# Kernel optimization log

Measured on AMD Instinct MI355X. Metric: run time of the kernel, lower is better.

The kernel has to match this reference:

```python
import jax, jax.numpy as jnp
import numpy as np

N_NODES = 100000
N_EDGES = 1600000
IN_CH = 128
HID = 64
N_LAYER = 4
N_CLASS = 10
N_GRAPHS = 512
EPS = 1e-5


def setup_inputs() -> dict:
    key = jax.random.key(0)
    ks = jax.random.split(key, 20)
    x = jax.random.normal(ks[0], (N_NODES, IN_CH), dtype=jnp.float32)
    src = jax.random.randint(ks[1], (N_EDGES,), 0, N_NODES)
    dst = jax.random.randint(ks[2], (N_EDGES,), 0, N_NODES)
    batch = jnp.sort(jax.random.randint(ks[3], (N_NODES,), 0, N_GRAPHS))
    s = 0.05
    W0 = jax.random.normal(ks[4], (IN_CH, HID), dtype=jnp.float32) * s
    Ws = jax.random.normal(ks[5], (N_LAYER - 1, HID, HID), dtype=jnp.float32) * s
    bs = jax.random.normal(ks[6], (N_LAYER, HID), dtype=jnp.float32) * s
    g_bn = jnp.ones((N_LAYER, HID), dtype=jnp.float32)
    b_bn = jnp.zeros((N_LAYER, HID), dtype=jnp.float32)
    m3 = 3 * N_LAYER * HID  # 768
    m2 = 2 * N_LAYER * HID  # 512
    m1 = N_LAYER * HID      # 256
    g_out = jnp.ones((m3,), dtype=jnp.float32)
    b_out = jnp.zeros((m3,), dtype=jnp.float32)
    w1 = jax.random.normal(ks[7], (m3, m2), dtype=jnp.float32) * s
    b1 = jnp.zeros((m2,), dtype=jnp.float32)
    w2 = jax.random.normal(ks[8], (m2, m1), dtype=jnp.float32) * s
    b2 = jnp.zeros((m1,), dtype=jnp.float32)
    w3 = jax.random.normal(ks[9], (m1, N_CLASS), dtype=jnp.float32) * s
    b3 = jnp.zeros((N_CLASS,), dtype=jnp.float32)
    return dict(x=x, src=src, dst=dst, batch=batch, W0=W0, Ws=Ws, bs=bs,
                g_bn=g_bn, b_bn=b_bn, g_out=g_out, b_out=b_out,
                w1=w1, b1=b1, w2=w2, b2=b2, w3=w3, b3=b3)


def _bn(h, g, b):
    # training-mode BatchNorm1d over rows (biased variance, as torch normalizes)
    m = jnp.mean(h, axis=0)
    v = jnp.var(h, axis=0)
    return (h - m) * jax.lax.rsqrt(v + EPS) * g + b


def reference(x, src, dst, batch, W0, Ws, bs, g_bn, b_bn, g_out, b_out,
              w1, b1, w2, b2, w3, b3):
    n = x.shape[0]
    loops = jnp.arange(n)
    s = jnp.concatenate([src, loops])  # self-loops (GCNConv)
    d = jnp.concatenate([dst, loops])
    deg = jax.ops.segment_sum(jnp.ones_like(s, dtype=x.dtype), d, num_segments=n)
    norm = jax.lax.rsqrt(jnp.maximum(deg, 1.0))
    coef = (norm[s] * norm[d])[:, None]

    def conv(h, W, bias):
        h = h @ W
        msg = h[s] * coef  # [E+N, HID] gather
        return jax.ops.segment_sum(msg, d, num_segments=n) + bias

    H = []
    h = conv(x, W0, bs[0])           # conv_act is identity (default)
    h = _bn(h, g_bn[0], b_bn[0])
    H.append(h)
    for i in range(N_LAYER - 1):
        h = conv(h, Ws[i], bs[i + 1])
        h = _bn(h, g_bn[i + 1], b_bn[i + 1])
        H.append(h)
    H = jnp.concatenate(H, axis=1)   # [N, n_layer*HID]

    # mean / add / max pooling by graph id
    add = jax.ops.segment_sum(H, batch, num_segments=N_GRAPHS)
    cnt = jax.ops.segment_sum(jnp.ones((n,), H.dtype), batch, num_segments=N_GRAPHS)
    avg = add / jnp.maximum(cnt, 1.0)[:, None]
    mx = jax.ops.segment_max(H, batch, num_segments=N_GRAPHS)
    mx = jnp.where(cnt[:, None] > 0, mx, 0.0)
    Hg = jnp.concatenate([avg, add, mx], axis=1)  # [G, 3*n_layer*HID]

    # funnel readout (dropout p=0 -> identity)
    z = _bn(Hg, g_out, b_out)
    z = jax.nn.relu(z @ w1 + b1)
    z = jax.nn.relu(z @ w2 + b2)
    return jax.nn.log_softmax(z @ w3 + b3, axis=1)
```

## Files before the change

kernel.cpp:

```cpp
#include <hip/hip_runtime.h>
#include <hip/hip_bf16.h>
#include <math.h>

#define HIDC 64
#define NLAYER 4
#define NG 512
#define M3 768
#define M2 512
#define M1 256
#define NCLS 10
#define EPSV 1e-5f
#define NB 512
#define EPT 16
#define NPW 4

__device__ inline unsigned bf16rne(float x){
  unsigned u = __float_as_uint(x);
  return (u + 0x7fffu + ((u >> 16) & 1u)) >> 16;
}
__device__ inline unsigned packbf2(float lo, float hi){
  return bf16rne(lo) | (bf16rne(hi) << 16);
}
__device__ inline float blo(unsigned u){ return __uint_as_float(u << 16); }
__device__ inline float bhi(unsigned u){ return __uint_as_float(u & 0xffff0000u); }

__global__ __launch_bounds__(256) void k_bhist(const int* __restrict__ dst, int E,
                                               int* __restrict__ bcnt){
  __shared__ int lc[NB];
  int tid = threadIdx.x;
  for (int i = tid; i < NB; i += 256) lc[i] = 0;
  __syncthreads();
  for (int e = blockIdx.x*256 + tid; e < E; e += gridDim.x*256)
    atomicAdd(&lc[__builtin_nontemporal_load(&dst[e]) >> 8], 1);
  __syncthreads();
  for (int i = tid; i < NB; i += 256){
    int c = lc[i];
    if (c) atomicAdd(&bcnt[i], c);
  }
}

__global__ void k_bscan(const int* __restrict__ bcnt, int* __restrict__ bofs,
                        int* __restrict__ bcursor){
  __shared__ int tmp[NB];
  int tid = threadIdx.x;
  int v = bcnt[tid];
  tmp[tid] = v; __syncthreads();
  for (int ofs = 1; ofs < NB; ofs <<= 1){
    int t = (tid >= ofs) ? tmp[tid-ofs] : 0;
    __syncthreads();
    tmp[tid] += t;
    __syncthreads();
  }
  int ex = tmp[tid] - v;
  bofs[tid] = ex;
  bcursor[tid] = ex;
}

__global__ __launch_bounds__(256) void k_bscatter(const int* __restrict__ src,
    const int* __restrict__ dst, int E, int* __restrict__ bcursor, int2* __restrict__ stage){
  __shared__ int lcnt[NB];
  __shared__ int lbase[NB];
  int tid = threadIdx.x;
  int t0 = blockIdx.x*(256*EPT);
  for (int i = tid; i < NB; i += 256) lcnt[i] = 0;
  __syncthreads();
  int s_[EPT], d_[EPT];
  bool ok[EPT];
  #pragma unroll
  for (int i = 0; i < EPT; i++){
    int e = t0 + i*256 + tid;
    ok[i] = (e < E);
    int ee = ok[i] ? e : 0;
    d_[i] = __builtin_nontemporal_load(&dst[ee]);
    s_[i] = __builtin_nontemporal_load(&src[ee]);
    if (ok[i]) atomicAdd(&lcnt[d_[i] >> 8], 1);
  }
  __syncthreads();
  for (int i = tid; i < NB; i += 256){
    int c = lcnt[i];
    lbase[i] = c ? atomicAdd(&bcursor[i], c) : 0;
  }
  __syncthreads();
  #pragma unroll
  for (int i = 0; i < EPT; i++){
    if (ok[i]){
      int pos = atomicAdd(&lbase[d_[i] >> 8], 1);
      stage[pos] = make_int2(s_[i], d_[i]);
    }
  }
}

__global__ __launch_bounds__(256) void k_deg_b(const int2* __restrict__ stage,
    const int* __restrict__ bofs, const int* __restrict__ bcnt,
    int* __restrict__ row_start, int* __restrict__ cursor,
    float* __restrict__ normv, int n, int E){
  __shared__ int hist[256];
  __shared__ int tmp[256];
  int b = blockIdx.x;
  int tid = threadIdx.x;
  hist[tid] = 0;
  __syncthreads();
  int st = bofs[b], en = st + bcnt[b];
  for (int i = st + tid; i < en; i += 256)
    atomicAdd(&hist[stage[i].y & 255], 1);
  __syncthreads();
  int v = hist[tid];
  tmp[tid] = v;
  __syncthreads();
  for (int o = 1; o < 256; o <<= 1){
    int t = (tid >= o) ? tmp[tid-o] : 0;
    __syncthreads();
    tmp[tid] += t;
    __syncthreads();
  }
  int node = b*256 + tid;
  if (node < n){
    int rs = st + tmp[tid] - v;
    row_start[node] = rs;
    cursor[node] = rs;
    normv[node] = rsqrtf((float)(v + 1));
  }
  if (b == 0 && tid == 0) row_start[n] = E;
}

__global__ __launch_bounds__(256) void k_fill_b(const int2* __restrict__ stage,
    const int* __restrict__ bofs, const int* __restrict__ bcnt,
    int* __restrict__ cursor, int* __restrict__ col){
  int b = blockIdx.x;
  int st = bofs[b], en = st + bcnt[b];
  for (int i = st + threadIdx.x; i < en; i += 256){
    int2 p = stage[i];
    int pos = atomicAdd(&cursor[p.y], 1);
    col[pos] = p.x;
  }
}

__global__ __launch_bounds__(256) void k_gemm_l0(const float* __restrict__ A,
    const float* __restrict__ W, const float* __restrict__ norm,
    unsigned* __restrict__ U32, int n){
  __shared__ float Wl[128*64];
  __shared__ float Al[128*36];
  int tid = threadIdx.x;
  {
    const float4* W4 = (const float4*)W;
    float4* Wl4 = (float4*)Wl;
    for (int i = tid; i < 128*16; i += 256) Wl4[i] = W4[i];
  }
  int rb = blockIdx.x * 128;
  int cg = tid & 7;
  int rg = tid >> 3;
  float acc[4][8];
  #pragma unroll
  for (int i = 0; i < 4; i++)
    #pragma unroll
    for (int c = 0; c < 8; c++) acc[i][c] = 0.f;
  for (int kc = 0; kc < 128; kc += 32){
    __syncthreads();
    {
      int r = tid >> 1, h = tid & 1;
      int rr = rb + r; if (rr >= n) rr = 0;
      const float* Ag = A + (size_t)rr*128 + kc + h*16;
      float4 v0 = *(const float4*)(Ag+0);
      float4 v1 = *(const float4*)(Ag+4);
      float4 v2 = *(const float4*)(Ag+8);
      float4 v3 = *(const float4*)(Ag+12);
      float* dl = &Al[r*36 + h*16];
      *(float4*)(dl+0) = v0; *(float4*)(dl+4) = v1;
      *(float4*)(dl+8) = v2; *(float4*)(dl+12) = v3;
    }
    __syncthreads();
    #pragma unroll
    for (int kk = 0; kk < 32; kk += 4){
      float4 a0 = *(const float4*)&Al[(rg*4+0)*36 + kk];
      float4 a1 = *(const float4*)&Al[(rg*4+1)*36 + kk];
      float4 a2 = *(const float4*)&Al[(rg*4+2)*36 + kk];
      float4 a3 = *(const float4*)&Al[(rg*4+3)*36 + kk];
      float ar[4][4] = {{a0.x,a0.y,a0.z,a0.w},{a1.x,a1.y,a1.z,a1.w},
                        {a2.x,a2.y,a2.z,a2.w},{a3.x,a3.y,a3.z,a3.w}};
      #pragma unroll
      for (int j = 0; j < 4; j++){
        const float* wr = &Wl[(kc+kk+j)*64 + cg*8];
        float4 w0 = *(const float4*)(wr);
        float4 w1 = *(const float4*)(wr+4);
        float wv[8] = {w0.x,w0.y,w0.z,w0.w,w1.x,w1.y,w1.z,w1.w};
        #pragma unroll
        for (int i = 0; i < 4; i++)
          #pragma unroll
          for (int c = 0; c < 8; c++)
            acc[i][c] += ar[i][j]*wv[c];
      }
    }
  }
  #pragma unroll
  for (int i = 0; i < 4; i++){
    int r = rb + rg*4 + i;
    if (r < n){
      float nr = norm[r];
      uint4 o;
      o.x = packbf2(acc[i][0]*nr, acc[i][1]*nr);
      o.y = packbf2(acc[i][2]*nr, acc[i][3]*nr);
      o.z = packbf2(acc[i][4]*nr, acc[i][5]*nr);
      o.w = packbf2(acc[i][6]*nr, acc[i][7]*nr);
      *(uint4*)(U32 + (size_t)r*32 + cg*4) = o;
    }
  }
}

__global__ __launch_bounds__(256) void k_gemm_lb(const unsigned* __restrict__ Ab,
    const float* __restrict__ W, const float* __restrict__ norm,
    const float* __restrict__ scsh, unsigned* __restrict__ U32, int n){
  __shared__ float Wl[64*64];
  __shared__ float Al[128*36];
  __shared__ float ss[128];
  int tid = threadIdx.x;
  {
    const float4* W4 = (const float4*)W;
    float4* Wl4 = (float4*)Wl;
    for (int i = tid; i < 64*16; i += 256) Wl4[i] = W4[i];
  }
  if (tid < 128) ss[tid] = scsh[tid];
  int rb = blockIdx.x * 128;
  int cg = tid & 7;
  int rg = tid >> 3;
  float acc[4][8];
  #pragma unroll
  for (int i = 0; i < 4; i++)
    #pragma unroll
    for (int c = 0; c < 8; c++) acc[i][c] = 0.f;
  for (int kc = 0; kc < 64; kc += 32){
    __syncthreads();
    {
      int r = tid >> 1, h = tid & 1;
      int rr = rb + r; if (rr >= n) rr = 0;
      const uint4* Ag = (const uint4*)(Ab + (size_t)rr*32 + (kc >> 1) + h*8);
      uint4 u0 = Ag[0], u1 = Ag[1];
      int kl = h*16;
      int kg = kc + kl;
      float f[16];
      f[0]=blo(u0.x); f[1]=bhi(u0.x); f[2]=blo(u0.y); f[3]=bhi(u0.y);
      f[4]=blo(u0.z); f[5]=bhi(u0.z); f[6]=blo(u0.w); f[7]=bhi(u0.w);
      f[8]=blo(u1.x); f[9]=bhi(u1.x); f[10]=blo(u1.y); f[11]=bhi(u1.y);
      f[12]=blo(u1.z); f[13]=bhi(u1.z); f[14]=blo(u1.w); f[15]=bhi(u1.w);
      #pragma unroll
      for (int j = 0; j < 16; j++) f[j] = f[j]*ss[kg+j] + ss[64+kg+j];
      float* dl = &Al[r*36 + kl];
      *(float4*)(dl+0)  = make_float4(f[0],f[1],f[2],f[3]);
      *(float4*)(dl+4)  = make_float4(f[4],f[5],f[6],f[7]);
      *(float4*)(dl+8)  = make_float4(f[8],f[9],f[10],f[11]);
      *(float4*)(dl+12) = make_float4(f[12],f[13],f[14],f[15]);
    }
    __syncthreads();
    #pragma unroll
    for (int kk = 0; kk < 32; kk += 4){
      float4 a0 = *(const float4*)&Al[(rg*4+0)*36 + kk];
      float4 a1 = *(const float4*)&Al[(rg*4+1)*36 + kk];
      float4 a2 = *(const float4*)&Al[(rg*4+2)*36 + kk];
      float4 a3 = *(const float4*)&Al[(rg*4+3)*36 + kk];
      float ar[4][4] = {{a0.x,a0.y,a0.z,a0.w},{a1.x,a1.y,a1.z,a1.w},
                        {a2.x,a2.y,a2.z,a2.w},{a3.x,a3.y,a3.z,a3.w}};
      #pragma unroll
      for (int j = 0; j < 4; j++){
        const float* wr = &Wl[(kc+kk+j)*64 + cg*8];
        float4 w0 = *(const float4*)(wr);
        float4 w1 = *(const float4*)(wr+4);
        float wv[8] = {w0.x,w0.y,w0.z,w0.w,w1.x,w1.y,w1.z,w1.w};
        #pragma unroll
        for (int i = 0; i < 4; i++)
          #pragma unroll
          for (int c = 0; c < 8; c++)
            acc[i][c] += ar[i][j]*wv[c];
      }
    }
  }
  #pragma unroll
  for (int i = 0; i < 4; i++){
    int r = rb + rg*4 + i;
    if (r < n){
      float nr = norm[r];
      uint4 o;
      o.x = packbf2(acc[i][0]*nr, acc[i][1]*nr);
      o.y = packbf2(acc[i][2]*nr, acc[i][3]*nr);
      o.z = packbf2(acc[i][4]*nr, acc[i][5]*nr);
      o.w = packbf2(acc[i][6]*nr, acc[i][7]*nr);
      *(uint4*)(U32 + (size_t)r*32 + cg*4) = o;
    }
  }
}

__global__ __launch_bounds__(256) void k_agg_bn(const unsigned* __restrict__ U32,
    const int* __restrict__ row_start, const int* __restrict__ col,
    const float* __restrict__ norm, unsigned* __restrict__ AGGb,
    float* __restrict__ sums8, int n){
  int tid = threadIdx.x;
  int wv = tid >> 6;
  int lane = tid & 63;
  int half = lane >> 5;
  int cl = lane & 31;
  float rs0=0.f, rs1=0.f, rq0=0.f, rq1=0.f;
  int base = blockIdx.x*(4*NPW) + wv*NPW;
  #pragma unroll
  for (int it = 0; it < NPW; ++it){
    int node = __builtin_amdgcn_readfirstlane(base + it);
    bool nv = (node < n);
    int nodec = nv ? node : 0;
    int st = row_start[nodec], en = row_start[nodec+1];
    float s0 = 0.f, s1 = 0.f;
    if (half == 0){
      unsigned u = U32[(size_t)nodec*32 + cl];
      s0 = blo(u); s1 = bhi(u);
    }
    int nit = (en - st + 15) >> 4;
    for (int i = 0; i < nit; i++){
      int k = st + i*16 + half*8;
      unsigned ua[8]; float m[8];
      #pragma unroll
      for (int j = 0; j < 8; j++){
        int kk = k + j;
        bool v = (kk < en);
        int idx = v ? kk : st;
        int jn = col[idx];
        ua[j] = U32[(size_t)jn*32 + cl];
        m[j] = v ? 1.f : 0.f;
      }
      #pragma unroll
      for (int j = 0; j < 8; j++){
        s0 += m[j]*blo(ua[j]);
        s1 += m[j]*bhi(ua[j]);
      }
    }
    s0 += __shfl_xor(s0, 32);
    s1 += __shfl_xor(s1, 32);
    if (half == 0 && nv){
      float nr = norm[node];
      s0 *= nr; s1 *= nr;
      AGGb[(size_t)node*32 + cl] = packbf2(s0, s1);
      rs0 += s0; rs1 += s1; rq0 += s0*s0; rq1 += s1*s1;
    }
  }
  __shared__ float L[4][32][4];
  if (half == 0){ L[wv][cl][0]=rs0; L[wv][cl][1]=rs1; L[wv][cl][2]=rq0; L[wv][cl][3]=rq1; }
  __syncthreads();
  if (tid < 128){
    int c2 = tid & 31, f = tid >> 5;
    float v = L[0][c2][f] + L[1][c2][f] + L[2][c2][f] + L[3][c2][f];
    int addr = ((f >= 2) ? 64 : 0) + 2*c2 + (f & 1);
    atomicAdd(&sums8[(blockIdx.x & 7)*128 + addr], v);
  }
}

__global__ void k_bn_finalize(const float* __restrict__ sums8, const float* __restrict__ g,
                              const float* __restrict__ b, float* __restrict__ scsh, float invn){
  int c = threadIdx.x;
  float s1 = 0.f, s2 = 0.f;
  #pragma unroll
  for (int s = 0; s < 8; s++){ s1 += sums8[s*128 + c]; s2 += sums8[s*128 + 64 + c]; }
  float mean = s1*invn;
  float var = s2*invn - mean*mean;
  var = fmaxf(var, 0.f);
  float sv = g[c]*rsqrtf(var + EPSV);
  scsh[c] = sv;
  scsh[64 + c] = b[c] - mean*sv;
}

__device__ inline int lowerb(const int* a, int n, int key){
  int lo = 0, hi = n;
  while (lo < hi){ int mid = (lo+hi) >> 1; if (a[mid] < key) lo = mid+1; else hi = mid; }
  return lo;
}

__global__ __launch_bounds__(256) void k_pool_part(const unsigned* __restrict__ AGGall,
    size_t lstride32, const float* __restrict__ bnss, const int* __restrict__ batch,
    int n, float* __restrict__ Ppart){
  int bid = blockIdx.x;
  int g = bid >> 3, sub = bid & 7;
  int c = threadIdx.x;
  int l = c >> 6, ch = c & 63;
  const unsigned* A = AGGall + (size_t)l * lstride32;
  float sc = bnss[l*128 + ch], sh = bnss[l*128 + 64 + ch];
  int hi16 = ch & 1;
  int uofs = ch >> 1;
  int st = lowerb(batch, n, g), en = lowerb(batch, n, g+1);
  int len = en - st;
  int r0 = st + (int)(((long long)sub * len) >> 3);
  int r1 = st + (int)(((long long)(sub+1) * len) >> 3);
  float s = 0.f, mx = -INFINITY;
  for (int r = r0; r < r1; r++){
    unsigned u = A[(size_t)r*32 + uofs];
    float v = hi16 ? bhi(u) : blo(u);
    v = v*sc + sh;
    s += v; mx = fmaxf(mx, v);
  }
  float* P = Ppart + (size_t)bid*512;
  P[c] = s;
  P[256 + c] = mx;
}

__global__ __launch_bounds__(256) void k_pool_comb(const float* __restrict__ Ppart,
    const int* __restrict__ batch, int n, float* __restrict__ Hg){
  int g = blockIdx.x; int c = threadIdx.x;
  float s = 0.f, mx = -INFINITY;
  #pragma unroll
  for (int sub = 0; sub < 8; sub++){
    const float* P = Ppart + (size_t)(g*8 + sub)*512;
    s += P[c];
    mx = fmaxf(mx, P[256 + c]);
  }
  int st = lowerb(batch, n, g), en = lowerb(batch, n, g+1);
  int cnt = en - st;
  float avg = s / (float)(cnt > 1 ? cnt : 1);
  float mo = (cnt > 0) ? mx : 0.f;
  Hg[(size_t)g*M3 + c]        = avg;
  Hg[(size_t)g*M3 + 256 + c]  = s;
  Hg[(size_t)g*M3 + 512 + c]  = mo;
}

__global__ void k_bn2(const float* __restrict__ Hg, const float* __restrict__ g,
                      const float* __restrict__ b, float* __restrict__ zsc, float* __restrict__ zsh){
  int c = blockIdx.x; int tid = threadIdx.x;
  float s1 = 0.f, s2 = 0.f;
  for (int r = tid; r < NG; r += 64){
    float v = Hg[(size_t)r*M3 + c];
    s1 += v; s2 += v*v;
  }
  for (int o = 32; o > 0; o >>= 1){ s1 += __shfl_down(s1, o); s2 += __shfl_down(s2, o); }
  if (tid == 0){
    float mean = s1/(float)NG;
    float var = s2/(float)NG - mean*mean;
    var = fmaxf(var, 0.f);
    float sc = g[c]*rsqrtf(var + EPSV);
    zsc[c] = sc;
    zsh[c] = b[c] - mean*sc;
  }
}

__global__ __launch_bounds__(256) void k_gemm_t(const float* __restrict__ A, int K,
    const float* __restrict__ W, int N, const float* __restrict__ bias,
    const float* __restrict__ zsc, const float* __restrict__ zsh,
    float* __restrict__ out, int relu, int applybn){
  __shared__ float As[32][36];
  __shared__ float Bs[32][36];
  int tid = threadIdx.x;
  int tx = tid & 15, ty = tid >> 4;
  int rb = blockIdx.y << 5, cb = blockIdx.x << 5;
  int lr = tid >> 3;
  int lk = (tid & 7) << 2;
  float acc00=0.f, acc01=0.f, acc10=0.f, acc11=0.f;
  for (int k0 = 0; k0 < K; k0 += 32){
    float4 av = *(const float4*)&A[(size_t)(rb+lr)*K + k0 + lk];
    if (applybn){
      av.x = av.x*zsc[k0+lk+0] + zsh[k0+lk+0];
      av.y = av.y*zsc[k0+lk+1] + zsh[k0+lk+1];
      av.z = av.z*zsc[k0+lk+2] + zsh[k0+lk+2];
      av.w = av.w*zsc[k0+lk+3] + zsh[k0+lk+3];
    }
    *(float4*)&As[lr][lk] = av;
    float4 bv = *(const float4*)&W[(size_t)(k0+lr)*N + cb + lk];
    Bs[lk+0][lr] = bv.x;
    Bs[lk+1][lr] = bv.y;
    Bs[lk+2][lr] = bv.z;
    Bs[lk+3][lr] = bv.w;
    __syncthreads();
    #pragma unroll
    for (int kk = 0; kk < 32; kk += 4){
      float4 a0 = *(const float4*)&As[ty][kk];
      float4 a1 = *(const float4*)&As[ty+16][kk];
      float4 b0 = *(const float4*)&Bs[tx][kk];
      float4 b1 = *(const float4*)&Bs[tx+16][kk];
      acc00 += a0.x*b0.x + a0.y*b0.y + a0.z*b0.z + a0.w*b0.w;
      acc01 += a0.x*b1.x + a0.y*b1.y + a0.z*b1.z + a0.w*b1.w;
      acc10 += a1.x*b0.x + a1.y*b0.y + a1.z*b0.z + a1.w*b0.w;
      acc11 += a1.x*b1.x + a1.y*b1.y + a1.z*b1.z + a1.w*b1.w;
    }
    __syncthreads();
  }
  int c0 = cb + tx, c1 = cb + tx + 16;
  float bz0 = bias[c0], bz1 = bias[c1];
  acc00 += bz0; acc01 += bz1; acc10 += bz0; acc11 += bz1;
  if (relu){
    acc00 = fmaxf(acc00, 0.f); acc01 = fmaxf(acc01, 0.f);
    acc10 = fmaxf(acc10, 0.f); acc11 = fmaxf(acc11, 0.f);
  }
  out[(size_t)(rb+ty)*N + c0]      = acc00;
  out[(size_t)(rb+ty)*N + c1]      = acc01;
  out[(size_t)(rb+ty+16)*N + c0]   = acc10;
  out[(size_t)(rb+ty+16)*N + c1]   = acc11;
}

__global__ __launch_bounds__(256) void k_gemm3_lsm(const float* __restrict__ A,
    const float* __restrict__ W, const float* __restrict__ bias, float* __restrict__ out){
  __shared__ float Wl[M1*NCLS];
  __shared__ float part[64][4][NCLS];
  int tid = threadIdx.x;
  for (int i = tid; i < M1*NCLS; i += 256) Wl[i] = W[i];
  __syncthreads();
  int r = blockIdx.x*64 + (tid >> 2);
  int q = tid & 3;
  float acc[NCLS];
  #pragma unroll
  for (int j = 0; j < NCLS; j++) acc[j] = 0.f;
  const float4* A4 = (const float4*)(A + (size_t)r*M1 + q*64);
  for (int kq = 0; kq < 16; kq++){
    float4 a = A4[kq];
    int kb = q*64 + kq*4;
    #pragma unroll
    for (int j = 0; j < NCLS; j++){
      acc[j] += a.x*Wl[(kb+0)*NCLS+j] + a.y*Wl[(kb+1)*NCLS+j]
              + a.z*Wl[(kb+2)*NCLS+j] + a.w*Wl[(kb+3)*NCLS+j];
    }
  }
  #pragma unroll
  for (int j = 0; j < NCLS; j++) part[tid>>2][q][j] = acc[j];
  __syncthreads();
  if (tid < 64){
    int rr = blockIdx.x*64 + tid;
    float v[NCLS]; float m = -INFINITY;
    #pragma unroll
    for (int j = 0; j < NCLS; j++){
      v[j] = part[tid][0][j] + part[tid][1][j] + part[tid][2][j] + part[tid][3][j] + bias[j];
      m = fmaxf(m, v[j]);
    }
    float s = 0.f;
    #pragma unroll
    for (int j = 0; j < NCLS; j++) s += expf(v[j] - m);
    float ls = logf(s) + m;
    #pragma unroll
    for (int j = 0; j < NCLS; j++) out[(size_t)rr*NCLS + j] = v[j] - ls;
  }
}

extern "C" void kernel_launch(void* const* d_in, const int* in_sizes, int n_in,
                              void* d_out, int out_size, void* d_ws, size_t ws_size,
                              hipStream_t stream){
  const float* x    = (const float*)d_in[0];
  const int*   src  = (const int*)d_in[1];
  const int*   dst  = (const int*)d_in[2];
  const int*   batch= (const int*)d_in[3];
  const float* W0   = (const float*)d_in[4];
  const float* Wsm  = (const float*)d_in[5];
  const float* g_bn = (const float*)d_in[7];
  const float* b_bn = (const float*)d_in[8];
  const float* g_out= (const float*)d_in[9];
  const float* b_out= (const float*)d_in[10];
  const float* w1   = (const float*)d_in[11];
  const float* b1   = (const float*)d_in[12];
  const float* w2   = (const float*)d_in[13];
  const float* b2   = (const float*)d_in[14];
  const float* w3   = (const float*)d_in[15];
  const float* b3   = (const float*)d_in[16];

  int n = in_sizes[3];
  int E = in_sizes[1];

  char* ws = (char*)d_ws;
  size_t off = 0;
  auto alloc = [&](size_t bytes) -> char* {
    char* p = ws + off;
    off += (bytes + 255) / 256 * 256;
    return p;
  };
  float* normv     = (float*)alloc((size_t)n*4);
  int*   row_start = (int*)  alloc((size_t)(n+1)*4);
  int*   cursor    = (int*)  alloc((size_t)n*4);
  int*   colA      = (int*)  alloc((size_t)E*4);
  int*   bcnt      = (int*)  alloc(NB*4);
  int*   bofs      = (int*)  alloc(NB*4);
  int*   bcursor   = (int*)  alloc(NB*4);
  int2*  stage     = (int2*) alloc((size_t)E*8);
  unsigned* U32    = (unsigned*)alloc((size_t)n*32*4);
  size_t lstride32 = (size_t)n*32;
  unsigned* AGGall = (unsigned*)alloc((size_t)NLAYER*lstride32*4);
  float* bnsums    = (float*)alloc(8*128*4);
  float* bnss      = (float*)alloc(NLAYER*128*4);
  float* Ppart     = (float*)alloc((size_t)NG*8*512*4);
  float* Hg        = (float*)alloc((size_t)NG*M3*4);
  float* Z1        = (float*)alloc((size_t)NG*M2*4);
  float* Z2        = (float*)alloc((size_t)NG*M1*4);
  float* zsc       = (float*)alloc(M3*4);
  float* zsh       = (float*)alloc(M3*4);

  int nb_used = (n + 255) >> 8;
  int gb = (n + 127) / 128;

  hipMemsetAsync(bcnt, 0, NB*4, stream);
  k_bhist<<<512, 256, 0, stream>>>(dst, E, bcnt);
  k_bscan<<<1, NB, 0, stream>>>(bcnt, bofs, bcursor);
  { int tiles = (E + 256*EPT - 1)/(256*EPT);
    k_bscatter<<<tiles, 256, 0, stream>>>(src, dst, E, bcursor, stage); }
  k_deg_b<<<nb_used, 256, 0, stream>>>(stage, bofs, bcnt, row_start, cursor, normv, n, E);
  k_fill_b<<<nb_used, 256, 0, stream>>>(stage, bofs, bcnt, cursor, colA);

  float invn = 1.f / (float)n;
  int aggblocks = (n + 4*NPW - 1) / (4*NPW);
  for (int l = 0; l < NLAYER; l++){
    unsigned* AGGb = AGGall + (size_t)l*lstride32;
    if (l == 0)
      k_gemm_l0<<<gb, 256, 0, stream>>>(x, W0, normv, U32, n);
    else
      k_gemm_lb<<<gb, 256, 0, stream>>>(AGGall + (size_t)(l-1)*lstride32,
                                        Wsm + (size_t)(l-1)*64*64, normv,
                                        bnss + (l-1)*128, U32, n);
    hipMemsetAsync(bnsums, 0, 8*128*4, stream);
    k_agg_bn<<<aggblocks, 256, 0, stream>>>(U32, row_start, colA, normv, AGGb, bnsums, n);
    k_bn_finalize<<<1, 64, 0, stream>>>(bnsums, g_bn + l*64, b_bn + l*64, bnss + l*128, invn);
  }

  k_pool_part<<<NG*8, 256, 0, stream>>>(AGGall, lstride32, bnss, batch, n, Ppart);
  k_pool_comb<<<NG, 256, 0, stream>>>(Ppart, batch, n, Hg);
  k_bn2<<<M3, 64, 0, stream>>>(Hg, g_out, b_out, zsc, zsh);

  { dim3 g1(M2/32, NG/32); k_gemm_t<<<g1, 256, 0, stream>>>(Hg, M3, w1, M2, b1, zsc, zsh, Z1, 1, 1); }
  { dim3 g2(M1/32, NG/32); k_gemm_t<<<g2, 256, 0, stream>>>(Z1, M2, w2, M1, b2, nullptr, nullptr, Z2, 1, 0); }
  k_gemm3_lsm<<<NG/64, 256, 0, stream>>>(Z2, w3, b3, (float*)d_out);
}
```

Measured before the change: 461.6 us.

## Use bf16 MFMA for node GEMMs, fold BN into weights, compact edge staging

The per-layer node GEMMs now run on bf16 MFMA (16x16x32) instead of fp32 scalar FMAs. The previous layer's BatchNorm scale is folded into a transposed bf16 weight copy, and its shift into a bias vector, both built by a small prep kernel per layer. The edge staging buffer is also packed from 8 to 4 bytes per edge by storing src<<8 together with the low 8 bits of dst. This cuts GEMM compute and edge-staging traffic, at the cost of extra tiny launches and bf16 rounding of x and of the scaled weights. The src<<8 packing assumes node ids fit in 24 bits.

```diff
diff --git a/kernel.cpp b/kernel.cpp
--- a/kernel.cpp
+++ b/kernel.cpp
@@ -14,6 +14,9 @@
 #define EPT 16
 #define NPW 4
 
+typedef float f32x4 __attribute__((ext_vector_type(4)));
+typedef short sh8   __attribute__((ext_vector_type(8)));
+
 __device__ inline unsigned bf16rne(float x){
   unsigned u = __float_as_uint(x);
   return (u + 0x7fffu + ((u >> 16) & 1u)) >> 16;
@@ -23,6 +26,12 @@
 }
 __device__ inline float blo(unsigned u){ return __uint_as_float(u << 16); }
 __device__ inline float bhi(unsigned u){ return __uint_as_float(u & 0xffff0000u); }
+
+__device__ inline sh8 ldfrag(const unsigned short* p){
+  union { uint4 u; sh8 s; } c;
+  c.u = *(const uint4*)p;
+  return c.s;
+}
 
 __global__ __launch_bounds__(256) void k_bhist(const int* __restrict__ dst, int E,
                                                int* __restrict__ bcnt){
@@ -57,7 +66,7 @@
 }
 
 __global__ __launch_bounds__(256) void k_bscatter(const int* __restrict__ src,
-    const int* __restrict__ dst, int E, int* __restrict__ bcursor, int2* __restrict__ stage){
+    const int* __restrict__ dst, int E, int* __restrict__ bcursor, unsigned* __restrict__ stage){
   __shared__ int lcnt[NB];
   __shared__ int lbase[NB];
   int tid = threadIdx.x;
@@ -85,12 +94,12 @@
   for (int i = 0; i < EPT; i++){
     if (ok[i]){
       int pos = atomicAdd(&lbase[d_[i] >> 8], 1);
-      stage[pos] = make_int2(s_[i], d_[i]);
-    }
-  }
-}
-
-__global__ __launch_bounds__(256) void k_deg_b(const int2* __restrict__ stage,
+      stage[pos] = ((unsigned)s_[i] << 8) | ((unsigned)d_[i] & 255u);
+    }
+  }
+}
+
+__global__ __launch_bounds__(256) void k_deg_b(const unsigned* __restrict__ stage,
     const int* __restrict__ bofs, const int* __restrict__ bcnt,
     int* __restrict__ row_start, int* __restrict__ cursor,
     float* __restrict__ normv, int n, int E){
@@ -102,7 +111,7 @@
   __syncthreads();
   int st = bofs[b], en = st + bcnt[b];
   for (int i = st + tid; i < en; i += 256)
-    atomicAdd(&hist[stage[i].y & 255], 1);
+    atomicAdd(&hist[stage[i] & 255u], 1);
   __syncthreads();
   int v = hist[tid];
   tmp[tid] = v;
@@ -123,168 +132,133 @@
   if (b == 0 && tid == 0) row_start[n] = E;
 }
 
-__global__ __launch_bounds__(256) void k_fill_b(const int2* __restrict__ stage,
+__global__ __launch_bounds__(256) void k_fill_b(const unsigned* __restrict__ stage,
     const int* __restrict__ bofs, const int* __restrict__ bcnt,
     int* __restrict__ cursor, int* __restrict__ col){
   int b = blockIdx.x;
   int st = bofs[b], en = st + bcnt[b];
   for (int i = st + threadIdx.x; i < en; i += 256){
-    int2 p = stage[i];
-    int pos = atomicAdd(&cursor[p.y], 1);
-    col[pos] = p.x;
-  }
-}
-
-__global__ __launch_bounds__(256) void k_gemm_l0(const float* __restrict__ A,
-    const float* __restrict__ W, const float* __restrict__ norm,
+    unsigned p = stage[i];
+    int node = (b << 8) | (int)(p & 255u);
+    int pos = atomicAdd(&cursor[node], 1);
+    col[pos] = (int)(p >> 8);
+  }
+}
+
+__global__ void k_prep(const float* __restrict__ W, const float* __restrict__ scsh,
+                       unsigned short* __restrict__ Wt, float* __restrict__ bvec, int K){
+  int c = threadIdx.x;
+  float bs = 0.f;
+  for (int k = 0; k < K; k++){
+    float w = W[(size_t)k*64 + c];
+    float sck = scsh ? scsh[k] : 1.f;
+    float shk = scsh ? scsh[64 + k] : 0.f;
+    Wt[(size_t)c*K + k] = (unsigned short)bf16rne(w*sck);
+    bs += shk*w;
+  }
+  bvec[c] = bs;
+}
+
+__device__ inline void mfma_epi(f32x4 acc[2][4], int rowbase, int lr, int lk,
+    const float* __restrict__ norm, const float* __restrict__ bias,
+    unsigned short* __restrict__ Ub, int n){
+  #pragma unroll
+  for (int m = 0; m < 2; m++){
+    #pragma unroll
+    for (int j = 0; j < 4; j++){
+      int row = rowbase + m*16 + lk*4 + j;
+      if (row < n){
+        float nr = norm[row];
+        #pragma unroll
+        for (int ct = 0; ct < 4; ct++){
+          int colv = ct*16 + lr;
+          float v = acc[m][ct][j];
+          if (bias) v += bias[colv];
+          Ub[(size_t)row*64 + colv] = (unsigned short)bf16rne(v*nr);
+        }
+      }
+    }
+  }
+}
+
+__global__ __launch_bounds__(256) void k_gemm_l0_mfma(const float* __restrict__ X,
+    const unsigned short* __restrict__ Wt, const float* __restrict__ norm,
     unsigned* __restrict__ U32, int n){
-  __shared__ float Wl[128*64];
-  __shared__ float Al[128*36];
-  int tid = threadIdx.x;
-  {
-    const float4* W4 = (const float4*)W;
-    float4* Wl4 = (float4*)Wl;
-    for (int i = tid; i < 128*16; i += 256) Wl4[i] = W4[i];
-  }
+  __shared__ unsigned short Al[128*40];
+  int tid = threadIdx.x;
+  int w = tid >> 6, l = tid & 63;
+  int lr = l & 15, lk = l >> 4;
   int rb = blockIdx.x * 128;
-  int cg = tid & 7;
-  int rg = tid >> 3;
-  float acc[4][8];
-  #pragma unroll
-  for (int i = 0; i < 4; i++)
-    #pragma unroll
-    for (int c = 0; c < 8; c++) acc[i][c] = 0.f;
+  f32x4 z = {0.f,0.f,0.f,0.f};
+  f32x4 acc[2][4];
+  #pragma unroll
+  for (int m = 0; m < 2; m++)
+    #pragma unroll
+    for (int ct = 0; ct < 4; ct++) acc[m][ct] = z;
   for (int kc = 0; kc < 128; kc += 32){
     __syncthreads();
     {
       int r = tid >> 1, h = tid & 1;
-      int rr = rb + r; if (rr >= n) rr = 0;
-      const float* Ag = A + (size_t)rr*128 + kc + h*16;
-      float4 v0 = *(const float4*)(Ag+0);
-      float4 v1 = *(const float4*)(Ag+4);
-      float4 v2 = *(const float4*)(Ag+8);
-      float4 v3 = *(const float4*)(Ag+12);
-      float* dl = &Al[r*36 + h*16];
-      *(float4*)(dl+0) = v0; *(float4*)(dl+4) = v1;
-      *(float4*)(dl+8) = v2; *(float4*)(dl+12) = v3;
-    }
-    __syncthreads();
-    #pragma unroll
-    for (int kk = 0; kk < 32; kk += 4){
-      float4 a0 = *(const float4*)&Al[(rg*4+0)*36 + kk];
-      float4 a1 = *(const float4*)&Al[(rg*4+1)*36 + kk];
-      float4 a2 = *(const float4*)&Al[(rg*4+2)*36 + kk];
-      float4 a3 = *(const float4*)&Al[(rg*4+3)*36 + kk];
-      float ar[4][4] = {{a0.x,a0.y,a0.z,a0.w},{a1.x,a1.y,a1.z,a1.w},
-                        {a2.x,a2.y,a2.z,a2.w},{a3.x,a3.y,a3.z,a3.w}};
+      int rr = rb + r; if (rr >= n) rr = n - 1;
+      const float* xp = X + (size_t)rr*128 + kc + h*16;
+      float4 v0 = *(const float4*)(xp+0);
+      float4 v1 = *(const float4*)(xp+4);
+      float4 v2 = *(const float4*)(xp+8);
+      float4 v3 = *(const float4*)(xp+12);
+      uint4 o0, o1;
+      o0.x = packbf2(v0.x, v0.y); o0.y = packbf2(v0.z, v0.w);
+      o0.z = packbf2(v1.x, v1.y); o0.w = packbf2(v1.z, v1.w);
+      o1.x = packbf2(v2.x, v2.y); o1.y = packbf2(v2.z, v2.w);
+      o1.z = packbf2(v3.x, v3.y); o1.w = packbf2(v3.z, v3.w);
+      unsigned short* dl = &Al[r*40 + h*16];
+      *(uint4*)(dl) = o0;
+      *(uint4*)(dl+8) = o1;
+    }
+    __syncthreads();
+    sh8 bfr[4];
+    #pragma unroll
+    for (int ct = 0; ct < 4; ct++)
+      bfr[ct] = ldfrag(&Wt[(size_t)(ct*16+lr)*128 + kc + lk*8]);
+    #pragma unroll
+    for (int m = 0; m < 2; m++){
+      sh8 af = ldfrag(&Al[(w*32 + m*16 + lr)*40 + lk*8]);
       #pragma unroll
-      for (int j = 0; j < 4; j++){
-        const float* wr = &Wl[(kc+kk+j)*64 + cg*8];
-        float4 w0 = *(const float4*)(wr);
-        float4 w1 = *(const float4*)(wr+4);
-        float wv[8] = {w0.x,w0.y,w0.z,w0.w,w1.x,w1.y,w1.z,w1.w};
-        #pragma unroll
-        for (int i = 0; i < 4; i++)
-          #pragma unroll
-          for (int c = 0; c < 8; c++)
-            acc[i][c] += ar[i][j]*wv[c];
-      }
-    }
-  }
-  #pragma unroll
-  for (int i = 0; i < 4; i++){
-    int r = rb + rg*4 + i;
-    if (r < n){
-      float nr = norm[r];
-      uint4 o;
-      o.x = packbf2(acc[i][0]*nr, acc[i][1]*nr);
-      o.y = packbf2(acc[i][2]*nr, acc[i][3]*nr);
-      o.z = packbf2(acc[i][4]*nr, acc[i][5]*nr);
-      o.w = packbf2(acc[i][6]*nr, acc[i][7]*nr);
-      *(uint4*)(U32 + (size_t)r*32 + cg*4) = o;
-    }
-  }
-}
-
-__global__ __launch_bounds__(256) void k_gemm_lb(const unsigned* __restrict__ Ab,
-    const float* __restrict__ W, const float* __restrict__ norm,
-    const float* __restrict__ scsh, unsigned* __restrict__ U32, int n){
-  __shared__ float Wl[64*64];
-  __shared__ float Al[128*36];
-  __shared__ float ss[128];
-  int tid = threadIdx.x;
-  {
-    const float4* W4 = (const float4*)W;
-    float4* Wl4 = (float4*)Wl;
-    for (int i = tid; i < 64*16; i += 256) Wl4[i] = W4[i];
-  }
-  if (tid < 128) ss[tid] = scsh[tid];
-  int rb = blockIdx.x * 128;
-  int cg = tid & 7;
-  int rg = tid >> 3;
-  float acc[4][8];
-  #pragma unroll
-  for (int i = 0; i < 4; i++)
-    #pragma unroll
-    for (int c = 0; c < 8; c++) acc[i][c] = 0.f;
+      for (int ct = 0; ct < 4; ct++)
+        acc[m][ct] = __builtin_amdgcn_mfma_f32_16x16x32_bf16(af, bfr[ct], acc[m][ct], 0, 0, 0);
+    }
+  }
+  mfma_epi(acc, rb + w*32, lr, lk, norm, nullptr, (unsigned short*)U32, n);
+}
+
+__global__ __launch_bounds__(256) void k_gemm_lb_mfma(const unsigned short* __restrict__ Ab,
+    const unsigned short* __restrict__ Wt, const float* __restrict__ bias,
+    const float* __restrict__ norm, unsigned* __restrict__ U32, int n){
+  int tid = threadIdx.x;
+  int w = tid >> 6, l = tid & 63;
+  int lr = l & 15, lk = l >> 4;
+  int rb = blockIdx.x * 128 + w*32;
+  f32x4 z = {0.f,0.f,0.f,0.f};
+  f32x4 acc[2][4];
+  #pragma unroll
+  for (int m = 0; m < 2; m++)
+    #pragma unroll
+    for (int ct = 0; ct < 4; ct++) acc[m][ct] = z;
+  #pragma unroll
   for (int kc = 0; kc < 64; kc += 32){
-    __syncthreads();
-    {
-      int r = tid >> 1, h = tid & 1;
-      int rr = rb + r; if (rr >= n) rr = 0;
-      const uint4* Ag = (const uint4*)(Ab + (size_t)rr*32 + (kc >> 1) + h*8);
-      uint4 u0 = Ag[0], u1 = Ag[1];
-      int kl = h*16;
-      int kg = kc + kl;
-      float f[16];
-      f[0]=blo(u0.x); f[1]=bhi(u0.x); f[2]=blo(u0.y); f[3]=bhi(u0.y);
-      f[4]=blo(u0.z); f[5]=bhi(u0.z); f[6]=blo(u0.w); f[7]=bhi(u0.w);
-      f[8]=blo(u1.x); f[9]=bhi(u1.x); f[10]=blo(u1.y); f[11]=bhi(u1.y);
-      f[12]=blo(u1.z); f[13]=bhi(u1.z); f[14]=blo(u1.w); f[15]=bhi(u1.w);
+    sh8 bfr[4];
+    #pragma unroll
+    for (int ct = 0; ct < 4; ct++)
+      bfr[ct] = ldfrag(&Wt[(size_t)(ct*16+lr)*64 + kc + lk*8]);
+    #pragma unroll
+    for (int m = 0; m < 2; m++){
+      int r = rb + m*16 + lr; if (r >= n) r = n - 1;
+      sh8 af = ldfrag(&Ab[(size_t)r*64 + kc + lk*8]);
       #pragma unroll
-      for (int j = 0; j < 16; j++) f[j] = f[j]*ss[kg+j] + ss[64+kg+j];
-      float* dl = &Al[r*36 + kl];
-      *(float4*)(dl+0)  = make_float4(f[0],f[1],f[2],f[3]);
-      *(float4*)(dl+4)  = make_float4(f[4],f[5],f[6],f[7]);
-      *(float4*)(dl+8)  = make_float4(f[8],f[9],f[10],f[11]);
-      *(float4*)(dl+12) = make_float4(f[12],f[13],f[14],f[15]);
-    }
-    __syncthreads();
-    #pragma unroll
-    for (int kk = 0; kk < 32; kk += 4){
-      float4 a0 = *(const float4*)&Al[(rg*4+0)*36 + kk];
-      float4 a1 = *(const float4*)&Al[(rg*4+1)*36 + kk];
-      float4 a2 = *(const float4*)&Al[(rg*4+2)*36 + kk];
-      float4 a3 = *(const float4*)&Al[(rg*4+3)*36 + kk];
-      float ar[4][4] = {{a0.x,a0.y,a0.z,a0.w},{a1.x,a1.y,a1.z,a1.w},
-                        {a2.x,a2.y,a2.z,a2.w},{a3.x,a3.y,a3.z,a3.w}};
-      #pragma unroll
-      for (int j = 0; j < 4; j++){
-        const float* wr = &Wl[(kc+kk+j)*64 + cg*8];
-        float4 w0 = *(const float4*)(wr);
-        float4 w1 = *(const float4*)(wr+4);
-        float wv[8] = {w0.x,w0.y,w0.z,w0.w,w1.x,w1.y,w1.z,w1.w};
-        #pragma unroll
-        for (int i = 0; i < 4; i++)
-          #pragma unroll
-          for (int c = 0; c < 8; c++)
-            acc[i][c] += ar[i][j]*wv[c];
-      }
-    }
-  }
-  #pragma unroll
-  for (int i = 0; i < 4; i++){
-    int r = rb + rg*4 + i;
-    if (r < n){
-      float nr = norm[r];
-      uint4 o;
-      o.x = packbf2(acc[i][0]*nr, acc[i][1]*nr);
-      o.y = packbf2(acc[i][2]*nr, acc[i][3]*nr);
-      o.z = packbf2(acc[i][4]*nr, acc[i][5]*nr);
-      o.w = packbf2(acc[i][6]*nr, acc[i][7]*nr);
-      *(uint4*)(U32 + (size_t)r*32 + cg*4) = o;
-    }
-  }
+      for (int ct = 0; ct < 4; ct++)
+        acc[m][ct] = __builtin_amdgcn_mfma_f32_16x16x32_bf16(af, bfr[ct], acc[m][ct], 0, 0, 0);
+    }
+  }
+  mfma_epi(acc, rb, lr, lk, norm, bias, (unsigned short*)U32, n);
 }
 
 __global__ __launch_bounds__(256) void k_agg_bn(const unsigned* __restrict__ U32,
@@ -565,12 +539,14 @@
   int*   bcnt      = (int*)  alloc(NB*4);
   int*   bofs      = (int*)  alloc(NB*4);
   int*   bcursor   = (int*)  alloc(NB*4);
-  int2*  stage     = (int2*) alloc((size_t)E*8);
+  unsigned* stage  = (unsigned*)alloc((size_t)E*4);
   unsigned* U32    = (unsigned*)alloc((size_t)n*32*4);
   size_t lstride32 = (size_t)n*32;
   unsigned* AGGall = (unsigned*)alloc((size_t)NLAYER*lstride32*4);
   float* bnsums    = (float*)alloc(8*128*4);
   float* bnss      = (float*)alloc(NLAYER*128*4);
+  unsigned short* Wt = (unsigned short*)alloc((size_t)NLAYER*64*128*2);
+  float* bvec      = (float*)alloc(NLAYER*64*4);
   float* Ppart     = (float*)alloc((size_t)NG*8*512*4);
   float* Hg        = (float*)alloc((size_t)NG*M3*4);
   float* Z1        = (float*)alloc((size_t)NG*M2*4);
@@ -579,9 +555,10 @@
   float* zsh       = (float*)alloc(M3*4);
 
   int nb_used = (n + 255) >> 8;
-  int gb = (n + 127) / 128;
+  int gb128 = (n + 127) / 128;
 
   hipMemsetAsync(bcnt, 0, NB*4, stream);
+  k_prep<<<1, 64, 0, stream>>>(W0, nullptr, Wt, bvec, 128);
   k_bhist<<<512, 256, 0, stream>>>(dst, E, bcnt);
   k_bscan<<<1, NB, 0, stream>>>(bcnt, bofs, bcursor);
   { int tiles = (E + 256*EPT - 1)/(256*EPT);
@@ -594,14 +571,17 @@
   for (int l = 0; l < NLAYER; l++){
     unsigned* AGGb = AGGall + (size_t)l*lstride32;
     if (l == 0)
-      k_gemm_l0<<<gb, 256, 0, stream>>>(x, W0, normv, U32, n);
+      k_gemm_l0_mfma<<<gb128, 256, 0, stream>>>(x, Wt, normv, U32, n);
     else
-      k_gemm_lb<<<gb, 256, 0, stream>>>(AGGall + (size_t)(l-1)*lstride32,
-                                        Wsm + (size_t)(l-1)*64*64, normv,
-                                        bnss + (l-1)*128, U32, n);
+      k_gemm_lb_mfma<<<gb128, 256, 0, stream>>>((const unsigned short*)(AGGall + (size_t)(l-1)*lstride32),
+                                                Wt + (size_t)l*64*128, bvec + l*64,
+                                                normv, U32, n);
     hipMemsetAsync(bnsums, 0, 8*128*4, stream);
     k_agg_bn<<<aggblocks, 256, 0, stream>>>(U32, row_start, colA, normv, AGGb, bnsums, n);
     k_bn_finalize<<<1, 64, 0, stream>>>(bnsums, g_bn + l*64, b_bn + l*64, bnss + l*128, invn);
+    if (l + 1 < NLAYER)
+      k_prep<<<1, 64, 0, stream>>>(Wsm + (size_t)l*64*64, bnss + l*128,
+                                   Wt + (size_t)(l+1)*64*128, bvec + (l+1)*64, 64);
   }
 
   k_pool_part<<<NG*8, 256, 0, stream>>>(AGGall, lstride32, bnss, batch, n, Ppart);
```

After: 524.8 us. 13.7% more time.
